# Performance work log

Hardware: AMD Instinct MI355X
Metric: run time of the kernel (lower is better)

Reference implementation:

```python
import jax, jax.numpy as jnp
import numpy as np

B, T, D = 4, 4096, 1024
N, L = 2048, 768
H = 16
EPS = 1e-5

def layernorm(x, g, b):
    mu = jnp.mean(x, axis=-1, keepdims=True)
    var = jnp.mean((x - mu) ** 2, axis=-1, keepdims=True)
    return (x - mu) * jax.lax.rsqrt(var + EPS) * g + b

def setup_inputs() -> dict:
    key = jax.random.key(0)
    ks = jax.random.split(key, 8)
    s_d = 1.0 / np.sqrt(D)
    s_l = 1.0 / np.sqrt(L)
    return {
        "x1": jax.random.normal(ks[0], (B, T, D), jnp.float32),
        "x2": jax.random.normal(ks[1], (B, N, L), jnp.float32),
        "Wq": jax.random.normal(ks[2], (D, D), jnp.float32) * s_d,
        "bq": jnp.zeros((D,), jnp.float32),
        "Wk": jax.random.normal(ks[3], (L, D), jnp.float32) * s_l,
        "bk": jnp.zeros((D,), jnp.float32),
        "Wv": jax.random.normal(ks[4], (L, D), jnp.float32) * s_l,
        "bv": jnp.zeros((D,), jnp.float32),
        "Wh": jax.random.normal(ks[5], (D, D), jnp.float32) * s_d,
        "bh": jnp.zeros((D,), jnp.float32),
        "g1": jnp.ones((D,), jnp.float32),
        "b1": jnp.zeros((D,), jnp.float32),
        "g2": jnp.ones((L,), jnp.float32),
        "b2": jnp.zeros((L,), jnp.float32),
    }

def reference(x1, x2, Wq, bq, Wk, bk, Wv, bv, Wh, bh, g1, b1, g2, b2):
    nx1 = layernorm(x1, g1, b1)
    nx2 = layernorm(x2, g2, b2)
    q = (nx1 @ Wq + bq).reshape(B, T, H, D // H)
    k = (nx2 @ Wk + bk).reshape(B, N, H, D // H)
    v = (nx2 @ Wv + bv).reshape(B, N, H, D // H)
    q = jax.nn.softmax(q, axis=-1)
    k = jax.nn.softmax(k, axis=-1)
    # dropout p=0 -> identity
    attn = jnp.einsum('bnhd,bnhl->bhdl', k, v)          # [B,H,dh,dh]
    y = jnp.einsum('bthd,bhdl->bthl', q, attn).reshape(B, T, D)
    return x1 @ Wh + bh + y
```

## Files before the change

### kernel.cpp

```cpp
#include <hip/hip_runtime.h>


#define DEV __device__ __forceinline__

typedef unsigned short bf16_t;
typedef __attribute__((ext_vector_type(8))) __bf16 bf16x8;
typedef __attribute__((ext_vector_type(8))) unsigned short ushort8;
typedef __attribute__((ext_vector_type(4))) float f32x4;

DEV unsigned short f2bf(float f) {
  unsigned int u = __float_as_uint(f);
  unsigned int r = 0x7FFFu + ((u >> 16) & 1u);
  return (unsigned short)((u + r) >> 16);
}
DEV float bf2f(unsigned short u) { return __uint_as_float(((unsigned int)u) << 16); }

DEV void gld16(const void* g, void* l) {
  __builtin_amdgcn_global_load_lds((__attribute__((address_space(1))) void*)g,
                                   (__attribute__((address_space(3))) void*)l, 16, 0, 0);
}

__global__ __launch_bounds__(256) void wprep_kernel(
    const float* __restrict__ Wq, const float* __restrict__ Wk,
    const float* __restrict__ Wv, const float* __restrict__ Wh,
    bf16_t* __restrict__ WqT, bf16_t* __restrict__ WkT,
    bf16_t* __restrict__ WvT, bf16_t* __restrict__ WhT) {
  int t = blockIdx.x;
  const float* src; bf16_t* dst; int K;
  if (t < 1024)      { src = Wq; dst = WqT; K = 1024; }
  else if (t < 1792) { src = Wk; dst = WkT; K = 768;  t -= 1024; }
  else if (t < 2560) { src = Wv; dst = WvT; K = 768;  t -= 1792; }
  else               { src = Wh; dst = WhT; K = 1024; t -= 2560; }
  int tk = t >> 5, tn = t & 31;
  __shared__ float tile[32][33];
  int tx = threadIdx.x & 31, ty = threadIdx.x >> 5;
#pragma unroll
  for (int i = 0; i < 4; ++i) {
    int r = ty + i * 8;
    tile[r][tx] = src[(size_t)(tk * 32 + r) * 1024 + tn * 32 + tx];
  }
  __syncthreads();
#pragma unroll
  for (int i = 0; i < 4; ++i) {
    int r = ty + i * 8;
    dst[(size_t)(tn * 32 + r) * K + tk * 32 + tx] = f2bf(tile[tx][r]);
  }
}

__global__ __launch_bounds__(256) void ln1_kernel(
    const float* __restrict__ x1, const float* __restrict__ g1, const float* __restrict__ b1,
    bf16_t* __restrict__ nx1, bf16_t* __restrict__ x1b) {
  int row = blockIdx.x, tid = threadIdx.x;
  size_t base = (size_t)row * 1024;
  float4 xv = *(const float4*)&x1[base + tid * 4];
  float s  = xv.x + xv.y + xv.z + xv.w;
  float s2 = xv.x * xv.x + xv.y * xv.y + xv.z * xv.z + xv.w * xv.w;
#pragma unroll
  for (int off = 32; off >= 1; off >>= 1) {
    s  += __shfl_down(s, off);
    s2 += __shfl_down(s2, off);
  }
  __shared__ float red[8];
  int wid = tid >> 6;
  if ((tid & 63) == 0) { red[wid] = s; red[4 + wid] = s2; }
  __syncthreads();
  s  = red[0] + red[1] + red[2] + red[3];
  s2 = red[4] + red[5] + red[6] + red[7];
  float mu = s * (1.0f / 1024.0f);
  float var = s2 * (1.0f / 1024.0f) - mu * mu;
  float rs = rsqrtf(var + 1e-5f);
  float4 gv = *(const float4*)&g1[tid * 4];
  float4 bv = *(const float4*)&b1[tid * 4];
  ushort4 pn, px;
  pn.x = f2bf((xv.x - mu) * rs * gv.x + bv.x);
  pn.y = f2bf((xv.y - mu) * rs * gv.y + bv.y);
  pn.z = f2bf((xv.z - mu) * rs * gv.z + bv.z);
  pn.w = f2bf((xv.w - mu) * rs * gv.w + bv.w);
  px.x = f2bf(xv.x); px.y = f2bf(xv.y); px.z = f2bf(xv.z); px.w = f2bf(xv.w);
  *(ushort4*)&nx1[base + tid * 4] = pn;
  *(ushort4*)&x1b[base + tid * 4] = px;
}

__global__ __launch_bounds__(256) void ln2_kernel(
    const float* __restrict__ x2, const float* __restrict__ g2, const float* __restrict__ b2,
    bf16_t* __restrict__ nx2) {
  int row = blockIdx.x, tid = threadIdx.x;
  size_t base = (size_t)row * 768;
  float a0 = x2[base + tid], a1 = x2[base + tid + 256], a2 = x2[base + tid + 512];
  float s = a0 + a1 + a2;
  float s2 = a0 * a0 + a1 * a1 + a2 * a2;
#pragma unroll
  for (int off = 32; off >= 1; off >>= 1) {
    s  += __shfl_down(s, off);
    s2 += __shfl_down(s2, off);
  }
  __shared__ float red[8];
  int wid = tid >> 6;
  if ((tid & 63) == 0) { red[wid] = s; red[4 + wid] = s2; }
  __syncthreads();
  s  = red[0] + red[1] + red[2] + red[3];
  s2 = red[4] + red[5] + red[6] + red[7];
  float mu = s * (1.0f / 768.0f);
  float var = s2 * (1.0f / 768.0f) - mu * mu;
  float rs = rsqrtf(var + 1e-5f);
  nx2[base + tid]       = f2bf((a0 - mu) * rs * g2[tid]       + b2[tid]);
  nx2[base + tid + 256] = f2bf((a1 - mu) * rs * g2[tid + 256] + b2[tid + 256]);
  nx2[base + tid + 512] = f2bf((a2 - mu) * rs * g2[tid + 512] + b2[tid + 512]);
}

__global__ __launch_bounds__(256, 2) void gemm_qkv_kernel(
    const bf16_t* __restrict__ nx1, const bf16_t* __restrict__ WqT,
    const float* __restrict__ bq, bf16_t* __restrict__ qout,
    const bf16_t* __restrict__ nx2, const bf16_t* __restrict__ WkT,
    const float* __restrict__ bk, bf16_t* __restrict__ kout,
    const bf16_t* __restrict__ WvT, const float* __restrict__ bv,
    bf16_t* __restrict__ vout) {
  __shared__ bf16_t As[128 * 32];
  __shared__ bf16_t Bs[256 * 32];
  int id = blockIdx.x;
  const bf16_t *A, *BT; const float* bias; bf16_t* out;
  int K, bm, bn, do_softmax;
  if (id < 512) {
    A = nx1; BT = WqT; bias = bq; out = qout; K = 1024;
    bm = id & 127; bn = id >> 7; do_softmax = 1;
  } else if (id < 768) {
    id -= 512; A = nx2; BT = WkT; bias = bk; out = kout; K = 768;
    bm = id & 63; bn = id >> 6; do_softmax = 1;
  } else {
    id -= 768; A = nx2; BT = WvT; bias = bv; out = vout; K = 768;
    bm = id & 63; bn = id >> 6; do_softmax = 0;
  }
  int tid = threadIdx.x;
  int lane = tid & 63, wid = tid >> 6;
  int wm = wid & 1, wn = wid >> 1;
  int klane = (lane >> 4) * 8;

  f32x4 acc[4][8];
#pragma unroll
  for (int i = 0; i < 4; ++i)
#pragma unroll
    for (int j = 0; j < 8; ++j) acc[i][j] = {0.f, 0.f, 0.f, 0.f};

  int nk = K >> 5;
  const bf16_t* Ab = A  + (size_t)bm * 128 * K;
  const bf16_t* Bb = BT + (size_t)bn * 256 * K;
  for (int kt = 0; kt < nk; ++kt) {
    __syncthreads();
    {
      int c = tid;
      gld16(Ab + (size_t)(c >> 2) * K + kt * 32 + (c & 3) * 8, (void*)(As + c * 8));
      c = 256 + tid;
      gld16(Ab + (size_t)(c >> 2) * K + kt * 32 + (c & 3) * 8, (void*)(As + c * 8));
#pragma unroll
      for (int i = 0; i < 4; ++i) {
        c = i * 256 + tid;
        gld16(Bb + (size_t)(c >> 2) * K + kt * 32 + (c & 3) * 8, (void*)(Bs + c * 8));
      }
    }
    __syncthreads();
    bf16x8 af[4], bfr[8];
#pragma unroll
    for (int mi = 0; mi < 4; ++mi)
      af[mi] = *(const bf16x8*)&As[(wm * 64 + mi * 16 + (lane & 15)) * 32 + klane];
#pragma unroll
    for (int ni = 0; ni < 8; ++ni)
      bfr[ni] = *(const bf16x8*)&Bs[(wn * 128 + ni * 16 + (lane & 15)) * 32 + klane];
#pragma unroll
    for (int mi = 0; mi < 4; ++mi)
#pragma unroll
      for (int ni = 0; ni < 8; ++ni)
        acc[mi][ni] = __builtin_amdgcn_mfma_f32_16x16x32_bf16(af[mi], bfr[ni], acc[mi][ni], 0, 0, 0);
  }

  int colg0 = bn * 256 + wn * 128;
  float bvv[8];
#pragma unroll
  for (int ni = 0; ni < 8; ++ni) bvv[ni] = bias[colg0 + ni * 16 + (lane & 15)];
#pragma unroll
  for (int mi = 0; mi < 4; ++mi) {
#pragma unroll
    for (int r = 0; r < 4; ++r) {
      int row = bm * 128 + wm * 64 + mi * 16 + (lane >> 4) * 4 + r;
      float vx[8];
#pragma unroll
      for (int ni = 0; ni < 8; ++ni) vx[ni] = acc[mi][ni][r] + bvv[ni];
      if (do_softmax) {
#pragma unroll
        for (int g = 0; g < 2; ++g) {
          float ssum = 0.f;
#pragma unroll
          for (int j = 0; j < 4; ++j) { vx[g * 4 + j] = __expf(vx[g * 4 + j]); ssum += vx[g * 4 + j]; }
#pragma unroll
          for (int off = 1; off < 16; off <<= 1) ssum += __shfl_xor(ssum, off);
          float inv = 1.0f / ssum;
#pragma unroll
          for (int j = 0; j < 4; ++j) vx[g * 4 + j] *= inv;
        }
      }
#pragma unroll
      for (int ni = 0; ni < 8; ++ni)
        out[(size_t)row * 1024 + colg0 + ni * 16 + (lane & 15)] = f2bf(vx[ni]);
    }
  }
}

__global__ __launch_bounds__(256) void attn_partial_kernel(
    const bf16_t* __restrict__ kq, const bf16_t* __restrict__ vq,
    float* __restrict__ part) {
  int bh = blockIdx.x >> 3, c = blockIdx.x & 7;
  int b = bh >> 4, h = bh & 15;
  int tid = threadIdx.x;
  int td = tid & 15, tl = tid >> 4;
  __shared__ float ks[32][64];
  __shared__ float vs[32][64];
  float acc[4][4];
#pragma unroll
  for (int i = 0; i < 4; ++i)
#pragma unroll
    for (int j = 0; j < 4; ++j) acc[i][j] = 0.f;
  for (int s = 0; s < 8; ++s) {
    __syncthreads();
    int nr = tid >> 3, col = (tid & 7) * 8;
    int n = c * 256 + s * 32 + nr;
    size_t goff = ((size_t)(b * 2048 + n)) * 1024 + h * 64 + col;
    ushort8 lk = *(const ushort8*)&kq[goff];
    ushort8 lv = *(const ushort8*)&vq[goff];
#pragma unroll
    for (int j = 0; j < 8; ++j) {
      ks[nr][col + j] = bf2f(lk[j]);
      vs[nr][col + j] = bf2f(lv[j]);
    }
    __syncthreads();
#pragma unroll
    for (int nn = 0; nn < 32; ++nn) {
      float4 kv = *(const float4*)&ks[nn][td * 4];
      float4 vv = *(const float4*)&vs[nn][tl * 4];
      float ka[4] = {kv.x, kv.y, kv.z, kv.w};
      float va[4] = {vv.x, vv.y, vv.z, vv.w};
#pragma unroll
      for (int i = 0; i < 4; ++i)
#pragma unroll
        for (int j = 0; j < 4; ++j) acc[i][j] += ka[i] * va[j];
    }
  }
#pragma unroll
  for (int i = 0; i < 4; ++i)
#pragma unroll
    for (int j = 0; j < 4; ++j) {
      int d = td * 4 + i, l = tl * 4 + j;
      part[(((size_t)bh * 8 + c) * 64 + d) * 64 + l] = acc[i][j];
    }
}

__global__ __launch_bounds__(256) void attn_finalize_kernel(
    const float* __restrict__ part, bf16_t* __restrict__ attnT) {
  int bh = blockIdx.x, tid = threadIdx.x;
  for (int t = tid; t < 4096; t += 256) {
    int d = t >> 6, l = t & 63;
    float s = 0.f;
#pragma unroll
    for (int c = 0; c < 8; ++c)
      s += part[(((size_t)bh * 8 + c) * 64 + d) * 64 + l];
    attnT[((size_t)bh * 64 + l) * 64 + d] = f2bf(s);
  }
}

__global__ __launch_bounds__(256, 2) void gemm_final_kernel(
    const bf16_t* __restrict__ A, const bf16_t* __restrict__ WT,
    const float* __restrict__ bias, const bf16_t* __restrict__ qb,
    const bf16_t* __restrict__ attnT, float* __restrict__ out) {
  __shared__ bf16_t As[128 * 32];
  __shared__ bf16_t Bs[256 * 32];
  const int K = 1024;
  int tid = threadIdx.x;
  int bm = blockIdx.x, bn = blockIdx.y;
  int lane = tid & 63, wid = tid >> 6;
  int wm = wid & 1, wn = wid >> 1;
  int b = bm >> 5;
  int klane = (lane >> 4) * 8;

  f32x4 acc[4][8];
#pragma unroll
  for (int i = 0; i < 4; ++i)
#pragma unroll
    for (int j = 0; j < 8; ++j) acc[i][j] = {0.f, 0.f, 0.f, 0.f};

  const bf16_t* Ab = A  + (size_t)bm * 128 * K;
  const bf16_t* Bb = WT + (size_t)bn * 256 * K;
  for (int kt = 0; kt < 32; ++kt) {
    __syncthreads();
    {
      int c = tid;
      gld16(Ab + (size_t)(c >> 2) * K + kt * 32 + (c & 3) * 8, (void*)(As + c * 8));
      c = 256 + tid;
      gld16(Ab + (size_t)(c >> 2) * K + kt * 32 + (c & 3) * 8, (void*)(As + c * 8));
#pragma unroll
      for (int i = 0; i < 4; ++i) {
        c = i * 256 + tid;
        gld16(Bb + (size_t)(c >> 2) * K + kt * 32 + (c & 3) * 8, (void*)(Bs + c * 8));
      }
    }
    __syncthreads();
    bf16x8 af[4], bfr[8];
#pragma unroll
    for (int mi = 0; mi < 4; ++mi)
      af[mi] = *(const bf16x8*)&As[(wm * 64 + mi * 16 + (lane & 15)) * 32 + klane];
#pragma unroll
    for (int ni = 0; ni < 8; ++ni)
      bfr[ni] = *(const bf16x8*)&Bs[(wn * 128 + ni * 16 + (lane & 15)) * 32 + klane];
#pragma unroll
    for (int mi = 0; mi < 4; ++mi)
#pragma unroll
      for (int ni = 0; ni < 8; ++ni)
        acc[mi][ni] = __builtin_amdgcn_mfma_f32_16x16x32_bf16(af[mi], bfr[ni], acc[mi][ni], 0, 0, 0);
  }

  {
    int h0 = bn * 4 + wn * 2;
#pragma unroll
    for (int k2 = 0; k2 < 2; ++k2) {
      bf16x8 aq[2][4], bt[8];
#pragma unroll
      for (int g = 0; g < 2; ++g)
#pragma unroll
        for (int mi = 0; mi < 4; ++mi)
          aq[g][mi] = *(const bf16x8*)(qb
              + (size_t)(bm * 128 + wm * 64 + mi * 16 + (lane & 15)) * 1024
              + (h0 + g) * 64 + k2 * 32 + klane);
#pragma unroll
      for (int ni = 0; ni < 8; ++ni)
        bt[ni] = *(const bf16x8*)(attnT
            + ((size_t)(b * 16 + h0 + (ni >> 2)) * 64 + (ni & 3) * 16 + (lane & 15)) * 64
            + k2 * 32 + klane);
#pragma unroll
      for (int mi = 0; mi < 4; ++mi)
#pragma unroll
        for (int ni = 0; ni < 8; ++ni)
          acc[mi][ni] = __builtin_amdgcn_mfma_f32_16x16x32_bf16(aq[ni >> 2][mi], bt[ni], acc[mi][ni], 0, 0, 0);
    }
  }

  int colg0 = bn * 256 + wn * 128;
  float bvv[8];
#pragma unroll
  for (int ni = 0; ni < 8; ++ni) bvv[ni] = bias[colg0 + ni * 16 + (lane & 15)];
#pragma unroll
  for (int mi = 0; mi < 4; ++mi)
#pragma unroll
    for (int r = 0; r < 4; ++r) {
      int row = bm * 128 + wm * 64 + mi * 16 + (lane >> 4) * 4 + r;
#pragma unroll
      for (int ni = 0; ni < 8; ++ni)
        out[(size_t)row * 1024 + colg0 + ni * 16 + (lane & 15)] = acc[mi][ni][r] + bvv[ni];
    }
}

extern "C" void kernel_launch(void* const* d_in, const int* in_sizes, int n_in,
                              void* d_out, int out_size, void* d_ws, size_t ws_size,
                              hipStream_t stream) {
  const float* x1 = (const float*)d_in[0];
  const float* x2 = (const float*)d_in[1];
  const float* Wq = (const float*)d_in[2];
  const float* bq = (const float*)d_in[3];
  const float* Wk = (const float*)d_in[4];
  const float* bk = (const float*)d_in[5];
  const float* Wv = (const float*)d_in[6];
  const float* bv = (const float*)d_in[7];
  const float* Wh = (const float*)d_in[8];
  const float* bh = (const float*)d_in[9];
  const float* g1 = (const float*)d_in[10];
  const float* b1 = (const float*)d_in[11];
  const float* g2 = (const float*)d_in[12];
  const float* b2 = (const float*)d_in[13];
  float* out = (float*)d_out;

  char* w = (char*)d_ws;
  bf16_t* nx1  = (bf16_t*)w; w += (size_t)16384 * 1024 * 2;
  bf16_t* x1b  = (bf16_t*)w; w += (size_t)16384 * 1024 * 2;
  bf16_t* nx2  = (bf16_t*)w; w += (size_t)8192 * 768 * 2;
  bf16_t* WqT  = (bf16_t*)w; w += (size_t)1024 * 1024 * 2;
  bf16_t* WkT  = (bf16_t*)w; w += (size_t)1024 * 768 * 2;
  bf16_t* WvT  = (bf16_t*)w; w += (size_t)1024 * 768 * 2;
  bf16_t* WhT  = (bf16_t*)w; w += (size_t)1024 * 1024 * 2;
  bf16_t* qb   = (bf16_t*)w; w += (size_t)16384 * 1024 * 2;
  bf16_t* kbuf = (bf16_t*)w; w += (size_t)8192 * 1024 * 2;
  bf16_t* vbuf = (bf16_t*)w; w += (size_t)8192 * 1024 * 2;
  float*  part = (float*)w;  w += (size_t)64 * 8 * 64 * 64 * 4;
  bf16_t* attnT = (bf16_t*)w; w += (size_t)64 * 64 * 64 * 2;

  wprep_kernel<<<dim3(3584), dim3(256), 0, stream>>>(Wq, Wk, Wv, Wh, WqT, WkT, WvT, WhT);
  ln1_kernel<<<dim3(16384), dim3(256), 0, stream>>>(x1, g1, b1, nx1, x1b);
  ln2_kernel<<<dim3(8192), dim3(256), 0, stream>>>(x2, g2, b2, nx2);
  gemm_qkv_kernel<<<dim3(1024), dim3(256), 0, stream>>>(
      nx1, WqT, bq, qb, nx2, WkT, bk, kbuf, WvT, bv, vbuf);
  attn_partial_kernel<<<dim3(512), dim3(256), 0, stream>>>(kbuf, vbuf, part);
  attn_finalize_kernel<<<dim3(64), dim3(256), 0, stream>>>(part, attnT);
  gemm_final_kernel<<<dim3(128, 4), dim3(256), 0, stream>>>(x1b, WhT, bh, qb, attnT, out);
}
```

Before: 327.9 us.

## Pre-swizzle operands into MFMA fragment layout and double-buffer GEMM B tiles

The weight-prep and layernorm kernels now write their bf16 outputs directly in a 16x32 fragment-tiled layout matching the MFMA operand order. This lets the GEMMs load A fragments straight from global memory into registers and stage only B through LDS. The B staging is double-buffered with manual waitcnt and barriers to overlap loads with MFMA work. The layernorm kernels process 16 rows per block through an LDS stash so they can emit the tiled layout. The trade-off is added complexity in hand-written waitcnt/barrier synchronisation, and per-wave A loads from global that bypass LDS sharing.

```diff
diff --git a/kernel.cpp b/kernel.cpp
--- a/kernel.cpp
+++ b/kernel.cpp
@@ -23,14 +23,14 @@
 __global__ __launch_bounds__(256) void wprep_kernel(
     const float* __restrict__ Wq, const float* __restrict__ Wk,
     const float* __restrict__ Wv, const float* __restrict__ Wh,
-    bf16_t* __restrict__ WqT, bf16_t* __restrict__ WkT,
-    bf16_t* __restrict__ WvT, bf16_t* __restrict__ WhT) {
+    bf16_t* __restrict__ Wqf, bf16_t* __restrict__ Wkf,
+    bf16_t* __restrict__ Wvf, bf16_t* __restrict__ Whf) {
   int t = blockIdx.x;
-  const float* src; bf16_t* dst; int K;
-  if (t < 1024)      { src = Wq; dst = WqT; K = 1024; }
-  else if (t < 1792) { src = Wk; dst = WkT; K = 768;  t -= 1024; }
-  else if (t < 2560) { src = Wv; dst = WvT; K = 768;  t -= 1792; }
-  else               { src = Wh; dst = WhT; K = 1024; t -= 2560; }
+  const float* src; bf16_t* dst; int KB;
+  if (t < 1024)      { src = Wq; dst = Wqf; KB = 32; }
+  else if (t < 1792) { src = Wk; dst = Wkf; KB = 24; t -= 1024; }
+  else if (t < 2560) { src = Wv; dst = Wvf; KB = 24; t -= 1792; }
+  else               { src = Wh; dst = Whf; KB = 32; t -= 2560; }
   int tk = t >> 5, tn = t & 31;
   __shared__ float tile[32][33];
   int tx = threadIdx.x & 31, ty = threadIdx.x >> 5;
@@ -40,100 +40,159 @@
     tile[r][tx] = src[(size_t)(tk * 32 + r) * 1024 + tn * 32 + tx];
   }
   __syncthreads();
-#pragma unroll
-  for (int i = 0; i < 4; ++i) {
-    int r = ty + i * 8;
-    dst[(size_t)(tn * 32 + r) * K + tk * 32 + tx] = f2bf(tile[tx][r]);
+  int tid = threadIdx.x;
+  if (tid < 128) {
+    int rt = tid >> 6, p = (tid >> 4) & 3, ri = tid & 15;
+    ushort8 v;
+#pragma unroll
+    for (int ko = 0; ko < 8; ++ko)
+      v[ko] = f2bf(tile[p * 8 + ko][rt * 16 + ri]);
+    size_t off = ((size_t)(tn * 2 + rt) * KB + tk) * 512 + p * 128 + ri * 8;
+    *(ushort8*)&dst[off] = v;
   }
 }
 
 __global__ __launch_bounds__(256) void ln1_kernel(
     const float* __restrict__ x1, const float* __restrict__ g1, const float* __restrict__ b1,
-    bf16_t* __restrict__ nx1, bf16_t* __restrict__ x1b) {
-  int row = blockIdx.x, tid = threadIdx.x;
-  size_t base = (size_t)row * 1024;
-  float4 xv = *(const float4*)&x1[base + tid * 4];
-  float s  = xv.x + xv.y + xv.z + xv.w;
-  float s2 = xv.x * xv.x + xv.y * xv.y + xv.z * xv.z + xv.w * xv.w;
-#pragma unroll
-  for (int off = 32; off >= 1; off >>= 1) {
-    s  += __shfl_down(s, off);
-    s2 += __shfl_down(s2, off);
-  }
-  __shared__ float red[8];
-  int wid = tid >> 6;
-  if ((tid & 63) == 0) { red[wid] = s; red[4 + wid] = s2; }
+    bf16_t* __restrict__ nx1f, bf16_t* __restrict__ x1f) {
+  __shared__ bf16_t stash[16 * 1032];
+  __shared__ float murs[16][2];
+  int rt = blockIdx.x, tid = threadIdx.x;
+  {
+    int rowl = tid >> 4, ci = tid & 15;
+    size_t base = ((size_t)rt * 16 + rowl) * 1024;
+    float s = 0.f, s2 = 0.f;
+#pragma unroll
+    for (int j = 0; j < 16; ++j) {
+      int k0 = ci * 4 + j * 64;
+      float4 f = *(const float4*)&x1[base + k0];
+      s += f.x + f.y + f.z + f.w;
+      s2 += f.x * f.x + f.y * f.y + f.z * f.z + f.w * f.w;
+      ushort4 u;
+      u.x = f2bf(f.x); u.y = f2bf(f.y); u.z = f2bf(f.z); u.w = f2bf(f.w);
+      *(ushort4*)&stash[rowl * 1032 + k0] = u;
+    }
+#pragma unroll
+    for (int off = 1; off < 16; off <<= 1) {
+      s  += __shfl_xor(s, off);
+      s2 += __shfl_xor(s2, off);
+    }
+    if (ci == 0) {
+      float mu = s * (1.0f / 1024.0f);
+      float var = s2 * (1.0f / 1024.0f) - mu * mu;
+      murs[rowl][0] = mu;
+      murs[rowl][1] = rsqrtf(var + 1e-5f);
+    }
+  }
   __syncthreads();
-  s  = red[0] + red[1] + red[2] + red[3];
-  s2 = red[4] + red[5] + red[6] + red[7];
-  float mu = s * (1.0f / 1024.0f);
-  float var = s2 * (1.0f / 1024.0f) - mu * mu;
-  float rs = rsqrtf(var + 1e-5f);
-  float4 gv = *(const float4*)&g1[tid * 4];
-  float4 bv = *(const float4*)&b1[tid * 4];
-  ushort4 pn, px;
-  pn.x = f2bf((xv.x - mu) * rs * gv.x + bv.x);
-  pn.y = f2bf((xv.y - mu) * rs * gv.y + bv.y);
-  pn.z = f2bf((xv.z - mu) * rs * gv.z + bv.z);
-  pn.w = f2bf((xv.w - mu) * rs * gv.w + bv.w);
-  px.x = f2bf(xv.x); px.y = f2bf(xv.y); px.z = f2bf(xv.z); px.w = f2bf(xv.w);
-  *(ushort4*)&nx1[base + tid * 4] = pn;
-  *(ushort4*)&x1b[base + tid * 4] = px;
+  {
+    int ri = tid & 15, pg = tid >> 4;
+    float mu = murs[ri][0], rs = murs[ri][1];
+#pragma unroll
+    for (int t = 0; t < 8; ++t) {
+      int P = pg * 8 + t;
+      ushort8 raw = *(const ushort8*)&stash[ri * 1032 + P * 8];
+      float4 ga = *(const float4*)&g1[P * 8], gb = *(const float4*)&g1[P * 8 + 4];
+      float4 ba = *(const float4*)&b1[P * 8], bb = *(const float4*)&b1[P * 8 + 4];
+      float gv[8] = {ga.x, ga.y, ga.z, ga.w, gb.x, gb.y, gb.z, gb.w};
+      float bv[8] = {ba.x, ba.y, ba.z, ba.w, bb.x, bb.y, bb.z, bb.w};
+      ushort8 nv;
+#pragma unroll
+      for (int ko = 0; ko < 8; ++ko)
+        nv[ko] = f2bf((bf2f(raw[ko]) - mu) * rs * gv[ko] + bv[ko]);
+      size_t off = ((size_t)rt * 32 + (P >> 2)) * 512 + (P & 3) * 128 + ri * 8;
+      *(ushort8*)&nx1f[off] = nv;
+      *(ushort8*)&x1f[off] = raw;
+    }
+  }
 }
 
 __global__ __launch_bounds__(256) void ln2_kernel(
     const float* __restrict__ x2, const float* __restrict__ g2, const float* __restrict__ b2,
-    bf16_t* __restrict__ nx2) {
-  int row = blockIdx.x, tid = threadIdx.x;
-  size_t base = (size_t)row * 768;
-  float a0 = x2[base + tid], a1 = x2[base + tid + 256], a2 = x2[base + tid + 512];
-  float s = a0 + a1 + a2;
-  float s2 = a0 * a0 + a1 * a1 + a2 * a2;
-#pragma unroll
-  for (int off = 32; off >= 1; off >>= 1) {
-    s  += __shfl_down(s, off);
-    s2 += __shfl_down(s2, off);
-  }
-  __shared__ float red[8];
-  int wid = tid >> 6;
-  if ((tid & 63) == 0) { red[wid] = s; red[4 + wid] = s2; }
+    bf16_t* __restrict__ nx2f) {
+  __shared__ bf16_t stash[16 * 776];
+  __shared__ float murs[16][2];
+  int rt = blockIdx.x, tid = threadIdx.x;
+  {
+    int rowl = tid >> 4, ci = tid & 15;
+    size_t base = ((size_t)rt * 16 + rowl) * 768;
+    float s = 0.f, s2 = 0.f;
+#pragma unroll
+    for (int j = 0; j < 12; ++j) {
+      int k0 = ci * 4 + j * 64;
+      float4 f = *(const float4*)&x2[base + k0];
+      s += f.x + f.y + f.z + f.w;
+      s2 += f.x * f.x + f.y * f.y + f.z * f.z + f.w * f.w;
+      ushort4 u;
+      u.x = f2bf(f.x); u.y = f2bf(f.y); u.z = f2bf(f.z); u.w = f2bf(f.w);
+      *(ushort4*)&stash[rowl * 776 + k0] = u;
+    }
+#pragma unroll
+    for (int off = 1; off < 16; off <<= 1) {
+      s  += __shfl_xor(s, off);
+      s2 += __shfl_xor(s2, off);
+    }
+    if (ci == 0) {
+      float mu = s * (1.0f / 768.0f);
+      float var = s2 * (1.0f / 768.0f) - mu * mu;
+      murs[rowl][0] = mu;
+      murs[rowl][1] = rsqrtf(var + 1e-5f);
+    }
+  }
   __syncthreads();
-  s  = red[0] + red[1] + red[2] + red[3];
-  s2 = red[4] + red[5] + red[6] + red[7];
-  float mu = s * (1.0f / 768.0f);
-  float var = s2 * (1.0f / 768.0f) - mu * mu;
-  float rs = rsqrtf(var + 1e-5f);
-  nx2[base + tid]       = f2bf((a0 - mu) * rs * g2[tid]       + b2[tid]);
-  nx2[base + tid + 256] = f2bf((a1 - mu) * rs * g2[tid + 256] + b2[tid + 256]);
-  nx2[base + tid + 512] = f2bf((a2 - mu) * rs * g2[tid + 512] + b2[tid + 512]);
+  {
+    int ri = tid & 15, pg = tid >> 4;
+    float mu = murs[ri][0], rs = murs[ri][1];
+#pragma unroll
+    for (int t = 0; t < 6; ++t) {
+      int P = pg * 6 + t;
+      ushort8 raw = *(const ushort8*)&stash[ri * 776 + P * 8];
+      float4 ga = *(const float4*)&g2[P * 8], gb = *(const float4*)&g2[P * 8 + 4];
+      float4 ba = *(const float4*)&b2[P * 8], bb = *(const float4*)&b2[P * 8 + 4];
+      float gv[8] = {ga.x, ga.y, ga.z, ga.w, gb.x, gb.y, gb.z, gb.w};
+      float bv[8] = {ba.x, ba.y, ba.z, ba.w, bb.x, bb.y, bb.z, bb.w};
+      ushort8 nv;
+#pragma unroll
+      for (int ko = 0; ko < 8; ++ko)
+        nv[ko] = f2bf((bf2f(raw[ko]) - mu) * rs * gv[ko] + bv[ko]);
+      size_t off = ((size_t)rt * 24 + (P >> 2)) * 512 + (P & 3) * 128 + ri * 8;
+      *(ushort8*)&nx2f[off] = nv;
+    }
+  }
 }
 
 __global__ __launch_bounds__(256, 2) void gemm_qkv_kernel(
-    const bf16_t* __restrict__ nx1, const bf16_t* __restrict__ WqT,
+    const bf16_t* __restrict__ nx1f, const bf16_t* __restrict__ Wqf,
     const float* __restrict__ bq, bf16_t* __restrict__ qout,
-    const bf16_t* __restrict__ nx2, const bf16_t* __restrict__ WkT,
+    const bf16_t* __restrict__ nx2f, const bf16_t* __restrict__ Wkf,
     const float* __restrict__ bk, bf16_t* __restrict__ kout,
-    const bf16_t* __restrict__ WvT, const float* __restrict__ bv,
+    const bf16_t* __restrict__ Wvf, const float* __restrict__ bv,
     bf16_t* __restrict__ vout) {
-  __shared__ bf16_t As[128 * 32];
-  __shared__ bf16_t Bs[256 * 32];
+  __shared__ bf16_t Bs[2 * 16 * 512];
   int id = blockIdx.x;
   const bf16_t *A, *BT; const float* bias; bf16_t* out;
-  int K, bm, bn, do_softmax;
+  int nk, bm, bn, do_softmax;
   if (id < 512) {
-    A = nx1; BT = WqT; bias = bq; out = qout; K = 1024;
+    A = nx1f; BT = Wqf; bias = bq; out = qout; nk = 32;
     bm = id & 127; bn = id >> 7; do_softmax = 1;
   } else if (id < 768) {
-    id -= 512; A = nx2; BT = WkT; bias = bk; out = kout; K = 768;
+    id -= 512; A = nx2f; BT = Wkf; bias = bk; out = kout; nk = 24;
     bm = id & 63; bn = id >> 6; do_softmax = 1;
   } else {
-    id -= 768; A = nx2; BT = WvT; bias = bv; out = vout; K = 768;
+    id -= 768; A = nx2f; BT = Wvf; bias = bv; out = vout; nk = 24;
     bm = id & 63; bn = id >> 6; do_softmax = 0;
   }
-  int tid = threadIdx.x;
-  int lane = tid & 63, wid = tid >> 6;
+  int tid = threadIdx.x, lane = tid & 63, wid = tid >> 6;
   int wm = wid & 1, wn = wid >> 1;
-  int klane = (lane >> 4) * 8;
+
+  const bf16_t* ap[4];
+#pragma unroll
+  for (int mi = 0; mi < 4; ++mi)
+    ap[mi] = A + ((size_t)(bm * 8 + wm * 4 + mi) * nk) * 512 + lane * 8;
+  const bf16_t* sp[4];
+#pragma unroll
+  for (int i = 0; i < 4; ++i)
+    sp[i] = BT + ((size_t)(bn * 16 + wid * 4 + i) * nk) * 512 + lane * 8;
 
   f32x4 acc[4][8];
 #pragma unroll
@@ -141,35 +200,38 @@
 #pragma unroll
     for (int j = 0; j < 8; ++j) acc[i][j] = {0.f, 0.f, 0.f, 0.f};
 
-  int nk = K >> 5;
-  const bf16_t* Ab = A  + (size_t)bm * 128 * K;
-  const bf16_t* Bb = BT + (size_t)bn * 256 * K;
+  bf16x8 acur[4], anxt[4];
+#pragma unroll
+  for (int i = 0; i < 4; ++i)
+    gld16(sp[i], (void*)&Bs[(wid * 4 + i) * 512 + lane * 8]);
+#pragma unroll
+  for (int mi = 0; mi < 4; ++mi) acur[mi] = *(const bf16x8*)ap[mi];
+
   for (int kt = 0; kt < nk; ++kt) {
-    __syncthreads();
-    {
-      int c = tid;
-      gld16(Ab + (size_t)(c >> 2) * K + kt * 32 + (c & 3) * 8, (void*)(As + c * 8));
-      c = 256 + tid;
-      gld16(Ab + (size_t)(c >> 2) * K + kt * 32 + (c & 3) * 8, (void*)(As + c * 8));
-#pragma unroll
-      for (int i = 0; i < 4; ++i) {
-        c = i * 256 + tid;
-        gld16(Bb + (size_t)(c >> 2) * K + kt * 32 + (c & 3) * 8, (void*)(Bs + c * 8));
-      }
-    }
-    __syncthreads();
-    bf16x8 af[4], bfr[8];
+    int cb = kt & 1;
+    if (kt + 1 < nk) {
+      int nb = cb ^ 1;
+#pragma unroll
+      for (int i = 0; i < 4; ++i)
+        gld16(sp[i] + (kt + 1) * 512, (void*)&Bs[nb * 8192 + (wid * 4 + i) * 512 + lane * 8]);
+#pragma unroll
+      for (int mi = 0; mi < 4; ++mi) anxt[mi] = *(const bf16x8*)(ap[mi] + (kt + 1) * 512);
+      asm volatile("s_waitcnt vmcnt(8)\n\ts_barrier" ::: "memory");
+    } else {
+      asm volatile("s_waitcnt vmcnt(0)\n\ts_barrier" ::: "memory");
+    }
+    bf16x8 bfr[8];
+#pragma unroll
+    for (int ni = 0; ni < 8; ++ni)
+      bfr[ni] = *(const bf16x8*)&Bs[cb * 8192 + (wn * 8 + ni) * 512 + lane * 8];
 #pragma unroll
     for (int mi = 0; mi < 4; ++mi)
-      af[mi] = *(const bf16x8*)&As[(wm * 64 + mi * 16 + (lane & 15)) * 32 + klane];
-#pragma unroll
-    for (int ni = 0; ni < 8; ++ni)
-      bfr[ni] = *(const bf16x8*)&Bs[(wn * 128 + ni * 16 + (lane & 15)) * 32 + klane];
-#pragma unroll
-    for (int mi = 0; mi < 4; ++mi)
 #pragma unroll
       for (int ni = 0; ni < 8; ++ni)
-        acc[mi][ni] = __builtin_amdgcn_mfma_f32_16x16x32_bf16(af[mi], bfr[ni], acc[mi][ni], 0, 0, 0);
+        acc[mi][ni] = __builtin_amdgcn_mfma_f32_16x16x32_bf16(acur[mi], bfr[ni], acc[mi][ni], 0, 0, 0);
+    asm volatile("s_waitcnt lgkmcnt(0)\n\ts_barrier" ::: "memory");
+#pragma unroll
+    for (int mi = 0; mi < 4; ++mi) acur[mi] = anxt[mi];
   }
 
   int colg0 = bn * 256 + wn * 128;
@@ -266,12 +328,11 @@
 }
 
 __global__ __launch_bounds__(256, 2) void gemm_final_kernel(
-    const bf16_t* __restrict__ A, const bf16_t* __restrict__ WT,
+    const bf16_t* __restrict__ x1f, const bf16_t* __restrict__ Whf,
     const float* __restrict__ bias, const bf16_t* __restrict__ qb,
     const bf16_t* __restrict__ attnT, float* __restrict__ out) {
-  __shared__ bf16_t As[128 * 32];
-  __shared__ bf16_t Bs[256 * 32];
-  const int K = 1024;
+  __shared__ bf16_t Bs[2 * 16 * 512];
+  const int nk = 32;
   int tid = threadIdx.x;
   int bm = blockIdx.x, bn = blockIdx.y;
   int lane = tid & 63, wid = tid >> 6;
@@ -279,40 +340,53 @@
   int b = bm >> 5;
   int klane = (lane >> 4) * 8;
 
+  const bf16_t* ap[4];
+#pragma unroll
+  for (int mi = 0; mi < 4; ++mi)
+    ap[mi] = x1f + ((size_t)(bm * 8 + wm * 4 + mi) * nk) * 512 + lane * 8;
+  const bf16_t* sp[4];
+#pragma unroll
+  for (int i = 0; i < 4; ++i)
+    sp[i] = Whf + ((size_t)(bn * 16 + wid * 4 + i) * nk) * 512 + lane * 8;
+
   f32x4 acc[4][8];
 #pragma unroll
   for (int i = 0; i < 4; ++i)
 #pragma unroll
     for (int j = 0; j < 8; ++j) acc[i][j] = {0.f, 0.f, 0.f, 0.f};
 
-  const bf16_t* Ab = A  + (size_t)bm * 128 * K;
-  const bf16_t* Bb = WT + (size_t)bn * 256 * K;
-  for (int kt = 0; kt < 32; ++kt) {
-    __syncthreads();
-    {
-      int c = tid;
-      gld16(Ab + (size_t)(c >> 2) * K + kt * 32 + (c & 3) * 8, (void*)(As + c * 8));
-      c = 256 + tid;
-      gld16(Ab + (size_t)(c >> 2) * K + kt * 32 + (c & 3) * 8, (void*)(As + c * 8));
-#pragma unroll
-      for (int i = 0; i < 4; ++i) {
-        c = i * 256 + tid;
-        gld16(Bb + (size_t)(c >> 2) * K + kt * 32 + (c & 3) * 8, (void*)(Bs + c * 8));
-      }
-    }
-    __syncthreads();
-    bf16x8 af[4], bfr[8];
+  bf16x8 acur[4], anxt[4];
+#pragma unroll
+  for (int i = 0; i < 4; ++i)
+    gld16(sp[i], (void*)&Bs[(wid * 4 + i) * 512 + lane * 8]);
+#pragma unroll
+  for (int mi = 0; mi < 4; ++mi) acur[mi] = *(const bf16x8*)ap[mi];
+
+  for (int kt = 0; kt < nk; ++kt) {
+    int cb = kt & 1;
+    if (kt + 1 < nk) {
+      int nb = cb ^ 1;
+#pragma unroll
+      for (int i = 0; i < 4; ++i)
+        gld16(sp[i] + (kt + 1) * 512, (void*)&Bs[nb * 8192 + (wid * 4 + i) * 512 + lane * 8]);
+#pragma unroll
+      for (int mi = 0; mi < 4; ++mi) anxt[mi] = *(const bf16x8*)(ap[mi] + (kt + 1) * 512);
+      asm volatile("s_waitcnt vmcnt(8)\n\ts_barrier" ::: "memory");
+    } else {
+      asm volatile("s_waitcnt vmcnt(0)\n\ts_barrier" ::: "memory");
+    }
+    bf16x8 bfr[8];
+#pragma unroll
+    for (int ni = 0; ni < 8; ++ni)
+      bfr[ni] = *(const bf16x8*)&Bs[cb * 8192 + (wn * 8 + ni) * 512 + lane * 8];
 #pragma unroll
     for (int mi = 0; mi < 4; ++mi)
-      af[mi] = *(const bf16x8*)&As[(wm * 64 + mi * 16 + (lane & 15)) * 32 + klane];
-#pragma unroll
-    for (int ni = 0; ni < 8; ++ni)
-      bfr[ni] = *(const bf16x8*)&Bs[(wn * 128 + ni * 16 + (lane & 15)) * 32 + klane];
-#pragma unroll
-    for (int mi = 0; mi < 4; ++mi)
 #pragma unroll
       for (int ni = 0; ni < 8; ++ni)
-        acc[mi][ni] = __builtin_amdgcn_mfma_f32_16x16x32_bf16(af[mi], bfr[ni], acc[mi][ni], 0, 0, 0);
+        acc[mi][ni] = __builtin_amdgcn_mfma_f32_16x16x32_bf16(acur[mi], bfr[ni], acc[mi][ni], 0, 0, 0);
+    asm volatile("s_waitcnt lgkmcnt(0)\n\ts_barrier" ::: "memory");
+#pragma unroll
+    for (int mi = 0; mi < 4; ++mi) acur[mi] = anxt[mi];
   }
 
   {
@@ -375,25 +449,25 @@
   float* out = (float*)d_out;
 
   char* w = (char*)d_ws;
-  bf16_t* nx1  = (bf16_t*)w; w += (size_t)16384 * 1024 * 2;
-  bf16_t* x1b  = (bf16_t*)w; w += (size_t)16384 * 1024 * 2;
-  bf16_t* nx2  = (bf16_t*)w; w += (size_t)8192 * 768 * 2;
-  bf16_t* WqT  = (bf16_t*)w; w += (size_t)1024 * 1024 * 2;
-  bf16_t* WkT  = (bf16_t*)w; w += (size_t)1024 * 768 * 2;
-  bf16_t* WvT  = (bf16_t*)w; w += (size_t)1024 * 768 * 2;
-  bf16_t* WhT  = (bf16_t*)w; w += (size_t)1024 * 1024 * 2;
+  bf16_t* nx1f = (bf16_t*)w; w += (size_t)16384 * 1024 * 2;
+  bf16_t* x1f  = (bf16_t*)w; w += (size_t)16384 * 1024 * 2;
+  bf16_t* nx2f = (bf16_t*)w; w += (size_t)8192 * 768 * 2;
+  bf16_t* Wqf  = (bf16_t*)w; w += (size_t)1024 * 1024 * 2;
+  bf16_t* Wkf  = (bf16_t*)w; w += (size_t)1024 * 768 * 2;
+  bf16_t* Wvf  = (bf16_t*)w; w += (size_t)1024 * 768 * 2;
+  bf16_t* Whf  = (bf16_t*)w; w += (size_t)1024 * 1024 * 2;
   bf16_t* qb   = (bf16_t*)w; w += (size_t)16384 * 1024 * 2;
   bf16_t* kbuf = (bf16_t*)w; w += (size_t)8192 * 1024 * 2;
   bf16_t* vbuf = (bf16_t*)w; w += (size_t)8192 * 1024 * 2;
   float*  part = (float*)w;  w += (size_t)64 * 8 * 64 * 64 * 4;
   bf16_t* attnT = (bf16_t*)w; w += (size_t)64 * 64 * 64 * 2;
 
-  wprep_kernel<<<dim3(3584), dim3(256), 0, stream>>>(Wq, Wk, Wv, Wh, WqT, WkT, WvT, WhT);
-  ln1_kernel<<<dim3(16384), dim3(256), 0, stream>>>(x1, g1, b1, nx1, x1b);
-  ln2_kernel<<<dim3(8192), dim3(256), 0, stream>>>(x2, g2, b2, nx2);
+  wprep_kernel<<<dim3(3584), dim3(256), 0, stream>>>(Wq, Wk, Wv, Wh, Wqf, Wkf, Wvf, Whf);
+  ln1_kernel<<<dim3(1024), dim3(256), 0, stream>>>(x1, g1, b1, nx1f, x1f);
+  ln2_kernel<<<dim3(512), dim3(256), 0, stream>>>(x2, g2, b2, nx2f);
   gemm_qkv_kernel<<<dim3(1024), dim3(256), 0, stream>>>(
-      nx1, WqT, bq, qb, nx2, WkT, bk, kbuf, WvT, bv, vbuf);
+      nx1f, Wqf, bq, qb, nx2f, Wkf, bk, kbuf, Wvf, bv, vbuf);
   attn_partial_kernel<<<dim3(512), dim3(256), 0, stream>>>(kbuf, vbuf, part);
   attn_finalize_kernel<<<dim3(64), dim3(256), 0, stream>>>(part, attnT);
-  gemm_final_kernel<<<dim3(128, 4), dim3(256), 0, stream>>>(x1b, WhT, bh, qb, attnT, out);
-}
+  gemm_final_kernel<<<dim3(128, 4), dim3(256), 0, stream>>>(x1f, Whf, bh, qb, attnT, out);
+}
```

Measured after the change: 316.0 us. 1.04x faster.
